# Kernel optimization log

Measured on AMD Instinct MI355X. Metric: run time of the kernel, lower is better.

Reference implementation:

```python
import jax, jax.numpy as jnp
import numpy as np

N, B, T, D = 4, 4, 512, 512
H, DK, DV = 8, 64, 64
LN_EPS = 1e-5


def setup_inputs() -> dict:
    key = jax.random.key(0)
    ks = jax.random.split(key, 5)
    s = 1.0 / np.sqrt(D)
    return {
        "x": jax.random.normal(ks[0], (N, B, T, D), jnp.float32),
        "Wq": jax.random.normal(ks[1], (D, H * DK), jnp.float32) * s,
        "bq": jnp.zeros((H * DK,), jnp.float32),
        "Wk": jax.random.normal(ks[2], (D, H * DK), jnp.float32) * s,
        "bk": jnp.zeros((H * DK,), jnp.float32),
        "Wv": jax.random.normal(ks[3], (D, H * DV), jnp.float32) * s,
        "bv": jnp.zeros((H * DV,), jnp.float32),
        "Wo": jax.random.normal(ks[4], (H * DV, D), jnp.float32) * (1.0 / np.sqrt(H * DV)),
        "bo": jnp.zeros((D,), jnp.float32),
        "gamma": jnp.ones((D,), jnp.float32),
        "beta": jnp.zeros((D,), jnp.float32),
    }


def reference(x, Wq, bq, Wk, bk, Wv, bv, Wo, bo, gamma, beta):
    # x: [N, B, T, D] -- N variables, each [B, T, D]
    n = x.shape[0]
    # Project once per variable (the torch code redundantly recomputes K/V per query var).
    q = (x @ Wq + bq).reshape(n, B, T, H, DK).transpose(0, 1, 3, 2, 4)  # [N,B,H,T,DK]
    k = (x @ Wk + bk).reshape(n, B, T, H, DK).transpose(0, 1, 3, 2, 4)  # [N,B,H,T,DK]
    v = (x @ Wv + bv).reshape(n, B, T, H, DV).transpose(0, 1, 3, 2, 4)  # [N,B,H,T,DV]
    # All-pairs attention: softmax over keys of EACH key-variable separately.
    scores = jnp.einsum('qbhtk,cbhsk->qcbhts', q, k) / np.sqrt(DK)  # [Nq,Nc,B,H,T,T]
    attn = jax.nn.softmax(scores, axis=-1)
    ctx = jnp.einsum('qcbhts,cbhsv->qcbhtv', attn, v)  # [Nq,Nc,B,H,T,DV]
    ctx = ctx.transpose(0, 1, 2, 4, 3, 5).reshape(n, n, B, T, H * DV)
    out = ctx @ Wo + bo                     # per-pair output projection
    out = out.sum(axis=1) / n               # average over key variables -> [N,B,T,D]
    res = x + out
    mu = res.mean(axis=-1, keepdims=True)
    var = res.var(axis=-1, keepdims=True)
    y = (res - mu) / jnp.sqrt(var + LN_EPS) * gamma + beta
    return y
```

## Files before the change

### kernel.cpp

```cpp
#include <hip/hip_runtime.h>


typedef __bf16 bf16x8 __attribute__((ext_vector_type(8)));
typedef __bf16 bf16x4 __attribute__((ext_vector_type(4)));
typedef short shortx4 __attribute__((ext_vector_type(4)));
typedef float floatx4 __attribute__((ext_vector_type(4)));
typedef float floatx16 __attribute__((ext_vector_type(16)));
typedef unsigned short ushortx8 __attribute__((ext_vector_type(8)));

static __device__ __forceinline__ unsigned short f2bf(float f) {
  union { __bf16 h; unsigned short u; } c; c.h = (__bf16)f; return c.u;
}
static __device__ __forceinline__ float bf2f(unsigned short u) {
  union { unsigned u32; float f; } c; c.u32 = ((unsigned)u) << 16; return c.f;
}

#define QSCALE 0.18033688011112042f
#define SHIFT2 (-17.312340489609306f)

__global__ __launch_bounds__(256) void prep(
    const float* __restrict__ Wq, const float* __restrict__ Wk,
    const float* __restrict__ Wv, const float* __restrict__ Wo,
    const float* __restrict__ x,
    unsigned short* __restrict__ wqkvT, unsigned short* __restrict__ woT,
    unsigned short* __restrict__ x_bf)
{
  const int bid = blockIdx.x;
  const int tid = threadIdx.x;
  if (bid < 256) {
    __shared__ unsigned short lds[64][65];
    const int z = bid >> 6, rest = bid & 63;
    const int k0 = (rest >> 3) * 64, n0 = (rest & 7) * 64;
    const float* W; unsigned short* T;
    if (z == 0)      { W = Wq; T = wqkvT; }
    else if (z == 1) { W = Wk; T = wqkvT + 262144; }
    else if (z == 2) { W = Wv; T = wqkvT + 524288; }
    else             { W = Wo; T = woT; }
    const int xx = tid & 63, yy = tid >> 6;
#pragma unroll
    for (int i = 0; i < 16; ++i) {
      const int row = yy * 16 + i;
      lds[row][xx] = f2bf(W[(size_t)(k0 + row) * 512 + n0 + xx]);
    }
    __syncthreads();
#pragma unroll
    for (int i = 0; i < 16; ++i) {
      const int nr = yy * 16 + i;
      T[(size_t)(n0 + nr) * 512 + k0 + xx] = lds[xx][nr];
    }
  } else {
    const int i = (bid - 256) * 256 + tid;
    const float4 a = ((const float4*)x)[i * 2];
    const float4 b = ((const float4*)x)[i * 2 + 1];
    ushortx8 o;
    o[0] = f2bf(a.x); o[1] = f2bf(a.y); o[2] = f2bf(a.z); o[3] = f2bf(a.w);
    o[4] = f2bf(b.x); o[5] = f2bf(b.y); o[6] = f2bf(b.z); o[7] = f2bf(b.w);
    *(ushortx8*)(x_bf + (size_t)i * 8) = o;
  }
}

__global__ __launch_bounds__(256) void gemm_qkv(
    const unsigned short* __restrict__ Xb,
    const unsigned short* __restrict__ BT,
    const float* __restrict__ bq, const float* __restrict__ bk,
    const float* __restrict__ bv,
    unsigned short* __restrict__ Qo, unsigned short* __restrict__ Ko,
    unsigned short* __restrict__ Vo)
{
  __shared__ __align__(16) unsigned short lA[128][72];
  __shared__ __align__(16) unsigned short lB[128][72];
  const int tid  = threadIdx.x;
  const int wv   = tid >> 6, lane = tid & 63;
  const int quad = lane >> 4, l16 = lane & 15;
  const int wm = wv >> 1, wn = wv & 1;
  const int m0  = blockIdx.x * 128;
  const int by  = blockIdx.y;
  const int n0g = by * 128;
  const int sel = by >> 2;
  const float* bias = (sel == 0) ? bq : (sel == 1) ? bk : bv;
  const float scale = (sel == 0) ? QSCALE : 1.0f;
  unsigned short* outp = (sel == 0) ? Qo : (sel == 1) ? Ko : Vo;

  floatx4 acc[4][4] = {};
  const int srow = tid >> 1, sc0 = (tid & 1) * 32;

  for (int kc = 0; kc < 512; kc += 64) {
    __syncthreads();
    const unsigned short* as = Xb + (size_t)(m0 + srow) * 512 + kc + sc0;
    const unsigned short* bs = BT + (size_t)(n0g + srow) * 512 + kc + sc0;
#pragma unroll
    for (int j = 0; j < 4; ++j) {
      *(bf16x8*)&lA[srow][sc0 + j * 8] = *(const bf16x8*)(as + j * 8);
      *(bf16x8*)&lB[srow][sc0 + j * 8] = *(const bf16x8*)(bs + j * 8);
    }
    __syncthreads();
    bf16x8 af[4][2];
#pragma unroll
    for (int ti = 0; ti < 4; ++ti) {
      af[ti][0] = *(const bf16x8*)&lA[wm * 64 + ti * 16 + l16][quad * 8];
      af[ti][1] = *(const bf16x8*)&lA[wm * 64 + ti * 16 + l16][32 + quad * 8];
    }
#pragma unroll
    for (int ni = 0; ni < 4; ++ni) {
      bf16x8 b0 = *(const bf16x8*)&lB[wn * 64 + ni * 16 + l16][quad * 8];
      bf16x8 b1 = *(const bf16x8*)&lB[wn * 64 + ni * 16 + l16][32 + quad * 8];
#pragma unroll
      for (int ti = 0; ti < 4; ++ti) {
        acc[ti][ni] = __builtin_amdgcn_mfma_f32_16x16x32_bf16(af[ti][0], b0, acc[ti][ni], 0, 0, 0);
        acc[ti][ni] = __builtin_amdgcn_mfma_f32_16x16x32_bf16(af[ti][1], b1, acc[ti][ni], 0, 0, 0);
      }
    }
  }

#pragma unroll
  for (int ni = 0; ni < 4; ++ni) {
    const int n = (n0g & 511) + wn * 64 + ni * 16 + l16;
    const float bvv = bias[n];
    const int hh = n >> 6, dk = n & 63;
#pragma unroll
    for (int ti = 0; ti < 4; ++ti) {
      const int mb = m0 + wm * 64 + ti * 16 + quad * 4;
#pragma unroll
      for (int r = 0; r < 4; ++r) {
        const int m = mb + r;
        const int nb = m >> 9, t = m & 511;
        const float v = (acc[ti][ni][r] + bvv) * scale;
        if (sel == 2)
          outp[((size_t)(nb * 8 + hh) * 64 + dk) * 512 + t] = f2bf(v);
        else
          outp[((size_t)(nb * 8 + hh) * 512 + t) * 64 + dk] = f2bf(v);
      }
    }
  }
}

__global__ __launch_bounds__(256) void gemm_out(
    const unsigned short* __restrict__ C0, const unsigned short* __restrict__ C1,
    const unsigned short* __restrict__ BT, float* __restrict__ Cout)
{
  __shared__ __align__(16) unsigned short lA[128][72];
  __shared__ __align__(16) unsigned short lB[128][72];
  const int tid  = threadIdx.x;
  const int wv   = tid >> 6, lane = tid & 63;
  const int quad = lane >> 4, l16 = lane & 15;
  const int wm = wv >> 1, wn = wv & 1;
  const int m0 = blockIdx.x * 128, n0 = blockIdx.y * 128;

  floatx4 acc[4][4] = {};
  const int srow = tid >> 1, sc0 = (tid & 1) * 32;

  for (int kc = 0; kc < 512; kc += 64) {
    __syncthreads();
    const size_t aoff = (size_t)(m0 + srow) * 512 + kc + sc0;
    const unsigned short* bs = BT + (size_t)(n0 + srow) * 512 + kc + sc0;
#pragma unroll
    for (int j = 0; j < 4; ++j) {
      ushortx8 a0 = *(const ushortx8*)(C0 + aoff + j * 8);
      ushortx8 a1 = *(const ushortx8*)(C1 + aoff + j * 8);
      ushortx8 o;
#pragma unroll
      for (int e = 0; e < 8; ++e) o[e] = f2bf(bf2f(a0[e]) + bf2f(a1[e]));
      *(ushortx8*)&lA[srow][sc0 + j * 8] = o;
      *(bf16x8*)&lB[srow][sc0 + j * 8] = *(const bf16x8*)(bs + j * 8);
    }
    __syncthreads();
    bf16x8 af[4][2];
#pragma unroll
    for (int ti = 0; ti < 4; ++ti) {
      af[ti][0] = *(const bf16x8*)&lA[wm * 64 + ti * 16 + l16][quad * 8];
      af[ti][1] = *(const bf16x8*)&lA[wm * 64 + ti * 16 + l16][32 + quad * 8];
    }
#pragma unroll
    for (int ni = 0; ni < 4; ++ni) {
      bf16x8 b0 = *(const bf16x8*)&lB[wn * 64 + ni * 16 + l16][quad * 8];
      bf16x8 b1 = *(const bf16x8*)&lB[wn * 64 + ni * 16 + l16][32 + quad * 8];
#pragma unroll
      for (int ti = 0; ti < 4; ++ti) {
        acc[ti][ni] = __builtin_amdgcn_mfma_f32_16x16x32_bf16(af[ti][0], b0, acc[ti][ni], 0, 0, 0);
        acc[ti][ni] = __builtin_amdgcn_mfma_f32_16x16x32_bf16(af[ti][1], b1, acc[ti][ni], 0, 0, 0);
      }
    }
  }

#pragma unroll
  for (int ni = 0; ni < 4; ++ni) {
    const int n = n0 + wn * 64 + ni * 16 + l16;
#pragma unroll
    for (int ti = 0; ti < 4; ++ti) {
      const int mb = m0 + wm * 64 + ti * 16 + quad * 4;
#pragma unroll
      for (int r = 0; r < 4; ++r)
        Cout[(size_t)(mb + r) * 512 + n] = acc[ti][ni][r];
    }
  }
}

__global__ __launch_bounds__(256) void flash_kernel(
    const unsigned short* __restrict__ Q,
    const unsigned short* __restrict__ K,
    const unsigned short* __restrict__ VT,
    unsigned short* __restrict__ CTX2)
{
  __shared__ __align__(16) unsigned short lK[2][64][72];
  __shared__ __align__(16) unsigned short lV[2][64][68];
  const int tid  = threadIdx.x;
  const int wv   = tid >> 6, lane = tid & 63;
  const int l32  = lane & 31, u = lane >> 5;

  const int lin  = blockIdx.x;
  const int xcd  = lin & 7, slot = lin >> 3;
  const int tile = slot & 3;
  const int nbh  = xcd * 16 + ((slot >> 2) & 15);
  const int cg   = slot >> 6;
  const int t0   = tile * 128;
  const int h = nbh & 7, nb = nbh >> 3, b = nb & 3;

  const unsigned short* qbase = Q + ((size_t)nbh * 512 + (t0 + wv * 32 + l32)) * 64;
  bf16x8 qf[4];
#pragma unroll
  for (int c16 = 0; c16 < 4; ++c16)
    qf[c16] = *(const bf16x8*)(qbase + c16 * 16 + u * 8);

  const int srow = tid >> 2, sc0 = (tid & 3) * 16;
  const unsigned short *kptr, *vptr;
  auto setptr = [&](int it) {
    const int c = cg * 2 + (it >> 3), s0 = (it & 7) * 64;
    const size_t kvbh = (size_t)((c * 4 + b) * 8 + h);
    kptr = K  + kvbh * (512 * 64) + (size_t)(s0 + srow) * 64 + sc0;
    vptr = VT + kvbh * (64 * 512) + (size_t)srow * 512 + s0 + sc0;
  };
  bf16x8 rk0, rk1, rv0, rv1;
  auto loadregs = [&]() {
    rk0 = *(const bf16x8*)kptr; rk1 = *(const bf16x8*)(kptr + 8);
    rv0 = *(const bf16x8*)vptr; rv1 = *(const bf16x8*)(vptr + 8);
  };
  auto writebuf = [&](int p) {
    *(bf16x8*)&lK[p][srow][sc0]     = rk0;
    *(bf16x8*)&lK[p][srow][sc0 + 8] = rk1;
    union { bf16x8 v8; bf16x4 v4[2]; } c0, c1;
    c0.v8 = rv0; c1.v8 = rv1;
    *(bf16x4*)&lV[p][srow][sc0]      = c0.v4[0];
    *(bf16x4*)&lV[p][srow][sc0 + 4]  = c0.v4[1];
    *(bf16x4*)&lV[p][srow][sc0 + 8]  = c1.v4[0];
    *(bf16x4*)&lV[p][srow][sc0 + 12] = c1.v4[1];
  };

  setptr(0); loadregs();
  writebuf(0);
  setptr(1); loadregs();
  __syncthreads();

  floatx16 ofin0 = {}, ofin1 = {};
  floatx16 oc0, oc1;
  float lacc;

  for (int it = 0; it < 16; ++it) {
    const int cur = it & 1;
    const int st = it & 7;
    if (st == 0) { oc0 = floatx16{}; oc1 = floatx16{}; lacc = 0.f; }

    if (it < 15) writebuf(cur ^ 1);
    if (it < 14) { setptr(it + 2); loadregs(); }

    floatx16 sacc0, sacc1;
#pragma unroll
    for (int r = 0; r < 16; ++r) { sacc0[r] = SHIFT2; sacc1[r] = SHIFT2; }
#pragma unroll
    for (int c16 = 0; c16 < 4; ++c16) {
      bf16x8 ak0 = *(const bf16x8*)&lK[cur][l32][c16 * 16 + u * 8];
      bf16x8 ak1 = *(const bf16x8*)&lK[cur][32 + l32][c16 * 16 + u * 8];
      sacc0 = __builtin_amdgcn_mfma_f32_32x32x16_bf16(ak0, qf[c16], sacc0, 0, 0, 0);
      sacc1 = __builtin_amdgcn_mfma_f32_32x32x16_bf16(ak1, qf[c16], sacc1, 0, 0, 0);
    }

#pragma unroll
    for (int sb = 0; sb < 2; ++sb) {
      const floatx16& sa = sb ? sacc1 : sacc0;
#pragma unroll
      for (int c8 = 0; c8 < 4; ++c8) {
        float e0 = __builtin_amdgcn_exp2f(sa[4 * c8 + 0]);
        float e1 = __builtin_amdgcn_exp2f(sa[4 * c8 + 1]);
        float e2 = __builtin_amdgcn_exp2f(sa[4 * c8 + 2]);
        float e3 = __builtin_amdgcn_exp2f(sa[4 * c8 + 3]);
        lacc += (e0 + e1) + (e2 + e3);
        shortx4 pf;
        pf[0] = (short)f2bf(e0); pf[1] = (short)f2bf(e1);
        pf[2] = (short)f2bf(e2); pf[3] = (short)f2bf(e3);
        const int sloc = sb * 32 + c8 * 8 + u * 4;
        shortx4 vf0 = *(const shortx4*)&lV[cur][l32][sloc];
        shortx4 vf1 = *(const shortx4*)&lV[cur][32 + l32][sloc];
        oc0 = __builtin_amdgcn_mfma_f32_32x32x8bf16_1k(pf, vf0, oc0, 0, 0, 0);
        oc1 = __builtin_amdgcn_mfma_f32_32x32x8bf16_1k(pf, vf1, oc1, 0, 0, 0);
      }
    }

    if (st == 7) {
      float s = lacc;
      s += __shfl_xor(s, 32);
      const float inv = 1.0f / s;
#pragma unroll
      for (int r = 0; r < 16; ++r) {
        const int trow = (r & 3) + 8 * (r >> 2) + 4 * u;
        const float invr = __shfl(inv, trow);
        ofin0[r] += oc0[r] * invr;
        ofin1[r] += oc1[r] * invr;
      }
    }
    __syncthreads();
  }

  unsigned short* outp = CTX2 + (size_t)cg * (8192 * 512);
  const int mbase = nb * 512 + t0 + wv * 32;
#pragma unroll
  for (int r = 0; r < 16; ++r) {
    const int trow = (r & 3) + 8 * (r >> 2) + 4 * u;
    const size_t rowoff = (size_t)(mbase + trow) * 512 + h * 64;
    outp[rowoff + l32]      = f2bf(ofin0[r]);
    outp[rowoff + 32 + l32] = f2bf(ofin1[r]);
  }
}

__global__ __launch_bounds__(256) void ln_kernel(
    const float* __restrict__ x, const float* __restrict__ tmp,
    const float* __restrict__ bo, const float* __restrict__ gamma,
    const float* __restrict__ beta, float* __restrict__ out)
{
  const int row = blockIdx.x;
  const int t = threadIdx.x;
  const size_t base = (size_t)row * 512;
  const float r0 = x[base + t]       + 0.25f * tmp[base + t]       + bo[t];
  const float r1 = x[base + t + 256] + 0.25f * tmp[base + t + 256] + bo[t + 256];
  float s = r0 + r1, sq = r0 * r0 + r1 * r1;
#pragma unroll
  for (int off = 1; off < 64; off <<= 1) {
    s  += __shfl_xor(s, off);
    sq += __shfl_xor(sq, off);
  }
  __shared__ float ls[4], lq[4];
  const int wv = t >> 6, lane = t & 63;
  if (lane == 0) { ls[wv] = s; lq[wv] = sq; }
  __syncthreads();
  s  = ls[0] + ls[1] + ls[2] + ls[3];
  sq = lq[0] + lq[1] + lq[2] + lq[3];
  const float mu  = s * (1.0f / 512.0f);
  const float var = sq * (1.0f / 512.0f) - mu * mu;
  const float inv = rsqrtf(var + 1e-5f);
  out[base + t]       = (r0 - mu) * inv * gamma[t]       + beta[t];
  out[base + t + 256] = (r1 - mu) * inv * gamma[t + 256] + beta[t + 256];
}

extern "C" void kernel_launch(void* const* d_in, const int* in_sizes, int n_in,
                              void* d_out, int out_size, void* d_ws, size_t ws_size,
                              hipStream_t stream) {
  const float* x     = (const float*)d_in[0];
  const float* Wq    = (const float*)d_in[1];
  const float* bq    = (const float*)d_in[2];
  const float* Wk    = (const float*)d_in[3];
  const float* bk    = (const float*)d_in[4];
  const float* Wv    = (const float*)d_in[5];
  const float* bv    = (const float*)d_in[6];
  const float* Wo    = (const float*)d_in[7];
  const float* bo    = (const float*)d_in[8];
  const float* gamma = (const float*)d_in[9];
  const float* beta  = (const float*)d_in[10];
  float* out = (float*)d_out;

  char* w = (char*)d_ws;
  unsigned short* q_bf  = (unsigned short*)(w);
  unsigned short* k_bf  = (unsigned short*)(w + (size_t)8  * 1024 * 1024);
  unsigned short* vt_bf = (unsigned short*)(w + (size_t)16 * 1024 * 1024);
  unsigned short* x_bf  = (unsigned short*)(w + (size_t)24 * 1024 * 1024);
  unsigned short* ctx2  = (unsigned short*)(w + (size_t)24 * 1024 * 1024);
  unsigned short* wqkvT = (unsigned short*)(w + (size_t)40 * 1024 * 1024);
  unsigned short* woT   = wqkvT + 786432;
  float* tmp            = (float*)(w);

  prep<<<2304, 256, 0, stream>>>(Wq, Wk, Wv, Wo, x, wqkvT, woT, x_bf);
  gemm_qkv<<<dim3(64, 12), 256, 0, stream>>>(x_bf, wqkvT, bq, bk, bv,
                                             q_bf, k_bf, vt_bf);
  flash_kernel<<<1024, 256, 0, stream>>>(q_bf, k_bf, vt_bf, ctx2);
  gemm_out<<<dim3(64, 4), 256, 0, stream>>>(ctx2, ctx2 + (size_t)8192 * 512,
                                            woT, tmp);
  ln_kernel<<<8192, 256, 0, stream>>>(x, tmp, bo, gamma, beta, out);
}
```

Measured before the change: 197.6 us.

## Use direct global-to-LDS loads with XOR swizzle in flash kernel, vectorize layernorm

The flash kernel now stages K/V tiles with global_load_lds straight into unpadded, XOR-swizzled LDS buffers, replacing the register round-trip and its padding. The per-variable-pair context is written out after each phase and read back for accumulation instead of held in registers, which frees registers (launch bounds now ask for 4 blocks) at the cost of extra global traffic. The layernorm kernel moves to one wavefront per row with float4 loads and no shared-memory reduction. There is also a small index cleanup in gemm_qkv. Risks: the direct-to-LDS path has no explicit wait before the barrier, and the bf16 round-trip of the partial sum adds rounding error.

```diff
diff --git a/kernel.cpp b/kernel.cpp
--- a/kernel.cpp
+++ b/kernel.cpp
@@ -2,7 +2,6 @@
 
 
 typedef __bf16 bf16x8 __attribute__((ext_vector_type(8)));
-typedef __bf16 bf16x4 __attribute__((ext_vector_type(4)));
 typedef short shortx4 __attribute__((ext_vector_type(4)));
 typedef float floatx4 __attribute__((ext_vector_type(4)));
 typedef float floatx16 __attribute__((ext_vector_type(16)));
@@ -13,6 +12,12 @@
 }
 static __device__ __forceinline__ float bf2f(unsigned short u) {
   union { unsigned u32; float f; } c; c.u32 = ((unsigned)u) << 16; return c.f;
+}
+
+static __device__ __forceinline__ void gload16(const unsigned short* gp, unsigned short* lp) {
+  __builtin_amdgcn_global_load_lds(
+      (const __attribute__((address_space(1))) unsigned int*)gp,
+      (__attribute__((address_space(3))) unsigned int*)lp, 16, 0, 0);
 }
 
 #define QSCALE 0.18033688011112042f
@@ -74,9 +79,8 @@
   const int quad = lane >> 4, l16 = lane & 15;
   const int wm = wv >> 1, wn = wv & 1;
   const int m0  = blockIdx.x * 128;
-  const int by  = blockIdx.y;
-  const int n0g = by * 128;
-  const int sel = by >> 2;
+  const int n0g = blockIdx.y * 128;
+  const int sel = n0g >> 9;
   const float* bias = (sel == 0) ? bq : (sel == 1) ? bk : bv;
   const float scale = (sel == 0) ? QSCALE : 1.0f;
   unsigned short* outp = (sel == 0) ? Qo : (sel == 1) ? Ko : Vo;
@@ -195,14 +199,14 @@
   }
 }
 
-__global__ __launch_bounds__(256) void flash_kernel(
+__global__ __launch_bounds__(256, 4) void flash_kernel(
     const unsigned short* __restrict__ Q,
     const unsigned short* __restrict__ K,
     const unsigned short* __restrict__ VT,
     unsigned short* __restrict__ CTX2)
 {
-  __shared__ __align__(16) unsigned short lK[2][64][72];
-  __shared__ __align__(16) unsigned short lV[2][64][68];
+  __shared__ __align__(16) unsigned short lK[2][64][64];
+  __shared__ __align__(16) unsigned short lV[2][64][64];
   const int tid  = threadIdx.x;
   const int wv   = tid >> 6, lane = tid & 63;
   const int l32  = lane & 31, u = lane >> 5;
@@ -221,54 +225,44 @@
   for (int c16 = 0; c16 < 4; ++c16)
     qf[c16] = *(const bf16x8*)(qbase + c16 * 16 + u * 8);
 
-  const int srow = tid >> 2, sc0 = (tid & 3) * 16;
-  const unsigned short *kptr, *vptr;
-  auto setptr = [&](int it) {
+  const int lrow8 = lane >> 3;
+  const int glog  = (lane & 7) ^ lrow8;
+  const int m7    = l32 & 7;
+
+  auto issue = [&](int it, int p) {
     const int c = cg * 2 + (it >> 3), s0 = (it & 7) * 64;
     const size_t kvbh = (size_t)((c * 4 + b) * 8 + h);
-    kptr = K  + kvbh * (512 * 64) + (size_t)(s0 + srow) * 64 + sc0;
-    vptr = VT + kvbh * (64 * 512) + (size_t)srow * 512 + s0 + sc0;
+    const unsigned short* kb = K  + kvbh * (512 * 64) + (size_t)s0 * 64;
+    const unsigned short* vb = VT + kvbh * (64 * 512) + s0;
+#pragma unroll
+    for (int j = 0; j < 2; ++j) {
+      const int r8 = wv * 16 + j * 8;
+      gload16(kb + (size_t)(r8 + lrow8) * 64  + glog * 8, &lK[p][r8][0]);
+      gload16(vb + (size_t)(r8 + lrow8) * 512 + glog * 8, &lV[p][r8][0]);
+    }
   };
-  bf16x8 rk0, rk1, rv0, rv1;
-  auto loadregs = [&]() {
-    rk0 = *(const bf16x8*)kptr; rk1 = *(const bf16x8*)(kptr + 8);
-    rv0 = *(const bf16x8*)vptr; rv1 = *(const bf16x8*)(vptr + 8);
-  };
-  auto writebuf = [&](int p) {
-    *(bf16x8*)&lK[p][srow][sc0]     = rk0;
-    *(bf16x8*)&lK[p][srow][sc0 + 8] = rk1;
-    union { bf16x8 v8; bf16x4 v4[2]; } c0, c1;
-    c0.v8 = rv0; c1.v8 = rv1;
-    *(bf16x4*)&lV[p][srow][sc0]      = c0.v4[0];
-    *(bf16x4*)&lV[p][srow][sc0 + 4]  = c0.v4[1];
-    *(bf16x4*)&lV[p][srow][sc0 + 8]  = c1.v4[0];
-    *(bf16x4*)&lV[p][srow][sc0 + 12] = c1.v4[1];
-  };
-
-  setptr(0); loadregs();
-  writebuf(0);
-  setptr(1); loadregs();
+
+  issue(0, 0);
   __syncthreads();
 
-  floatx16 ofin0 = {}, ofin1 = {};
-  floatx16 oc0, oc1;
-  float lacc;
+  floatx16 oc0 = {}, oc1 = {};
+  float lacc = 0.f;
 
   for (int it = 0; it < 16; ++it) {
     const int cur = it & 1;
     const int st = it & 7;
     if (st == 0) { oc0 = floatx16{}; oc1 = floatx16{}; lacc = 0.f; }
 
-    if (it < 15) writebuf(cur ^ 1);
-    if (it < 14) { setptr(it + 2); loadregs(); }
+    if (it < 15) issue(it + 1, cur ^ 1);
 
     floatx16 sacc0, sacc1;
 #pragma unroll
     for (int r = 0; r < 16; ++r) { sacc0[r] = SHIFT2; sacc1[r] = SHIFT2; }
 #pragma unroll
     for (int c16 = 0; c16 < 4; ++c16) {
-      bf16x8 ak0 = *(const bf16x8*)&lK[cur][l32][c16 * 16 + u * 8];
-      bf16x8 ak1 = *(const bf16x8*)&lK[cur][32 + l32][c16 * 16 + u * 8];
+      const int pc = ((c16 * 2 + u) ^ m7) * 8;
+      bf16x8 ak0 = *(const bf16x8*)&lK[cur][l32][pc];
+      bf16x8 ak1 = *(const bf16x8*)&lK[cur][32 + l32][pc];
       sacc0 = __builtin_amdgcn_mfma_f32_32x32x16_bf16(ak0, qf[c16], sacc0, 0, 0, 0);
       sacc1 = __builtin_amdgcn_mfma_f32_32x32x16_bf16(ak1, qf[c16], sacc1, 0, 0, 0);
     }
@@ -286,9 +280,9 @@
         shortx4 pf;
         pf[0] = (short)f2bf(e0); pf[1] = (short)f2bf(e1);
         pf[2] = (short)f2bf(e2); pf[3] = (short)f2bf(e3);
-        const int sloc = sb * 32 + c8 * 8 + u * 4;
-        shortx4 vf0 = *(const shortx4*)&lV[cur][l32][sloc];
-        shortx4 vf1 = *(const shortx4*)&lV[cur][32 + l32][sloc];
+        const int pv = ((sb * 4 + c8) ^ m7) * 8 + u * 4;
+        shortx4 vf0 = *(const shortx4*)&lV[cur][l32][pv];
+        shortx4 vf1 = *(const shortx4*)&lV[cur][32 + l32][pv];
         oc0 = __builtin_amdgcn_mfma_f32_32x32x8bf16_1k(pf, vf0, oc0, 0, 0, 0);
         oc1 = __builtin_amdgcn_mfma_f32_32x32x8bf16_1k(pf, vf1, oc1, 0, 0, 0);
       }
@@ -298,25 +292,24 @@
       float s = lacc;
       s += __shfl_xor(s, 32);
       const float inv = 1.0f / s;
+      unsigned short* outp = CTX2 + (size_t)cg * (8192 * 512);
+      const int mbase = nb * 512 + t0 + wv * 32;
+      const int phase = it >> 3;
 #pragma unroll
       for (int r = 0; r < 16; ++r) {
         const int trow = (r & 3) + 8 * (r >> 2) + 4 * u;
         const float invr = __shfl(inv, trow);
-        ofin0[r] += oc0[r] * invr;
-        ofin1[r] += oc1[r] * invr;
-      }
-    }
-    __syncthreads();
-  }
-
-  unsigned short* outp = CTX2 + (size_t)cg * (8192 * 512);
-  const int mbase = nb * 512 + t0 + wv * 32;
-#pragma unroll
-  for (int r = 0; r < 16; ++r) {
-    const int trow = (r & 3) + 8 * (r >> 2) + 4 * u;
-    const size_t rowoff = (size_t)(mbase + trow) * 512 + h * 64;
-    outp[rowoff + l32]      = f2bf(ofin0[r]);
-    outp[rowoff + 32 + l32] = f2bf(ofin1[r]);
+        const size_t rowoff = (size_t)(mbase + trow) * 512 + h * 64;
+        float v0 = oc0[r] * invr, v1 = oc1[r] * invr;
+        if (phase == 1) {
+          v0 += bf2f(outp[rowoff + l32]);
+          v1 += bf2f(outp[rowoff + 32 + l32]);
+        }
+        outp[rowoff + l32]      = f2bf(v0);
+        outp[rowoff + 32 + l32] = f2bf(v1);
+      }
+    }
+    __syncthreads();
   }
 }
 
@@ -325,28 +318,43 @@
     const float* __restrict__ bo, const float* __restrict__ gamma,
     const float* __restrict__ beta, float* __restrict__ out)
 {
-  const int row = blockIdx.x;
-  const int t = threadIdx.x;
-  const size_t base = (size_t)row * 512;
-  const float r0 = x[base + t]       + 0.25f * tmp[base + t]       + bo[t];
-  const float r1 = x[base + t + 256] + 0.25f * tmp[base + t + 256] + bo[t + 256];
-  float s = r0 + r1, sq = r0 * r0 + r1 * r1;
+  const int wv   = threadIdx.x >> 6, lane = threadIdx.x & 63;
+  const int row  = blockIdx.x * 4 + wv;
+  const int col  = lane * 8;
+  const size_t base = (size_t)row * 512 + col;
+  const float4 x0 = *(const float4*)(x + base);
+  const float4 x1 = *(const float4*)(x + base + 4);
+  const float4 t0 = *(const float4*)(tmp + base);
+  const float4 t1 = *(const float4*)(tmp + base + 4);
+  const float4 b0 = *(const float4*)(bo + col);
+  const float4 b1 = *(const float4*)(bo + col + 4);
+  float r[8];
+  r[0] = x0.x + 0.25f * t0.x + b0.x;  r[1] = x0.y + 0.25f * t0.y + b0.y;
+  r[2] = x0.z + 0.25f * t0.z + b0.z;  r[3] = x0.w + 0.25f * t0.w + b0.w;
+  r[4] = x1.x + 0.25f * t1.x + b1.x;  r[5] = x1.y + 0.25f * t1.y + b1.y;
+  r[6] = x1.z + 0.25f * t1.z + b1.z;  r[7] = x1.w + 0.25f * t1.w + b1.w;
+  float s = 0.f, sq = 0.f;
+#pragma unroll
+  for (int j = 0; j < 8; ++j) { s += r[j]; sq += r[j] * r[j]; }
 #pragma unroll
   for (int off = 1; off < 64; off <<= 1) {
     s  += __shfl_xor(s, off);
     sq += __shfl_xor(sq, off);
   }
-  __shared__ float ls[4], lq[4];
-  const int wv = t >> 6, lane = t & 63;
-  if (lane == 0) { ls[wv] = s; lq[wv] = sq; }
-  __syncthreads();
-  s  = ls[0] + ls[1] + ls[2] + ls[3];
-  sq = lq[0] + lq[1] + lq[2] + lq[3];
   const float mu  = s * (1.0f / 512.0f);
   const float var = sq * (1.0f / 512.0f) - mu * mu;
   const float inv = rsqrtf(var + 1e-5f);
-  out[base + t]       = (r0 - mu) * inv * gamma[t]       + beta[t];
-  out[base + t + 256] = (r1 - mu) * inv * gamma[t + 256] + beta[t + 256];
+  const float4 g0 = *(const float4*)(gamma + col);
+  const float4 g1 = *(const float4*)(gamma + col + 4);
+  const float4 be0 = *(const float4*)(beta + col);
+  const float4 be1 = *(const float4*)(beta + col + 4);
+  float4 o0, o1;
+  o0.x = (r[0] - mu) * inv * g0.x + be0.x;  o0.y = (r[1] - mu) * inv * g0.y + be0.y;
+  o0.z = (r[2] - mu) * inv * g0.z + be0.z;  o0.w = (r[3] - mu) * inv * g0.w + be0.w;
+  o1.x = (r[4] - mu) * inv * g1.x + be1.x;  o1.y = (r[5] - mu) * inv * g1.y + be1.y;
+  o1.z = (r[6] - mu) * inv * g1.z + be1.z;  o1.w = (r[7] - mu) * inv * g1.w + be1.w;
+  *(float4*)(out + base)     = o0;
+  *(float4*)(out + base + 4) = o1;
 }
 
 extern "C" void kernel_launch(void* const* d_in, const int* in_sizes, int n_in,
@@ -381,5 +389,5 @@
   flash_kernel<<<1024, 256, 0, stream>>>(q_bf, k_bf, vt_bf, ctx2);
   gemm_out<<<dim3(64, 4), 256, 0, stream>>>(ctx2, ctx2 + (size_t)8192 * 512,
                                             woT, tmp);
-  ln_kernel<<<8192, 256, 0, stream>>>(x, tmp, bo, gamma, beta, out);
-}
+  ln_kernel<<<2048, 256, 0, stream>>>(x, tmp, bo, gamma, beta, out);
+}
```

After: 250.0 us. +26.5%, slower.

## Stage V transpose through LDS, store projection output in bf16, vectorize layernorm

Applied to the files above, without the earlier changes.

The V branch of the QKV GEMM now transposes its tile through shared memory and writes coalesced 16-byte rows, replacing strided scalar stores. The output-projection GEMM writes its intermediate in bf16 instead of fp32, halving that buffer's write and read traffic. The layernorm is rewritten so one wavefront handles one row with vectorized loads and stores and no block-level sync. The bf16 intermediate adds rounding error before the residual add and layernorm.

```diff
diff --git a/kernel.cpp b/kernel.cpp
--- a/kernel.cpp
+++ b/kernel.cpp
@@ -67,16 +67,16 @@
     unsigned short* __restrict__ Qo, unsigned short* __restrict__ Ko,
     unsigned short* __restrict__ Vo)
 {
-  __shared__ __align__(16) unsigned short lA[128][72];
-  __shared__ __align__(16) unsigned short lB[128][72];
+  __shared__ __align__(16) unsigned short sbuf[18432];
+  auto lA = (unsigned short (*)[72])sbuf;
+  auto lB = (unsigned short (*)[72])(sbuf + 9216);
   const int tid  = threadIdx.x;
   const int wv   = tid >> 6, lane = tid & 63;
   const int quad = lane >> 4, l16 = lane & 15;
   const int wm = wv >> 1, wn = wv & 1;
   const int m0  = blockIdx.x * 128;
-  const int by  = blockIdx.y;
-  const int n0g = by * 128;
-  const int sel = by >> 2;
+  const int n0g = blockIdx.y * 128;
+  const int sel = n0g >> 9;
   const float* bias = (sel == 0) ? bq : (sel == 1) ? bk : bv;
   const float scale = (sel == 0) ? QSCALE : 1.0f;
   unsigned short* outp = (sel == 0) ? Qo : (sel == 1) ? Ko : Vo;
@@ -112,31 +112,58 @@
     }
   }
 
-#pragma unroll
-  for (int ni = 0; ni < 4; ++ni) {
-    const int n = (n0g & 511) + wn * 64 + ni * 16 + l16;
-    const float bvv = bias[n];
+  if (sel != 2) {
+#pragma unroll
+    for (int ni = 0; ni < 4; ++ni) {
+      const int n = (n0g & 511) + wn * 64 + ni * 16 + l16;
+      const float bvv = bias[n];
+      const int hh = n >> 6, dk = n & 63;
+#pragma unroll
+      for (int ti = 0; ti < 4; ++ti) {
+        const int mb = m0 + wm * 64 + ti * 16 + quad * 4;
+#pragma unroll
+        for (int r = 0; r < 4; ++r) {
+          const int m = mb + r;
+          const int nb = m >> 9, t = m & 511;
+          outp[((size_t)(nb * 8 + hh) * 512 + t) * 64 + dk] =
+              f2bf((acc[ti][ni][r] + bvv) * scale);
+        }
+      }
+    }
+  } else {
+    __syncthreads();
+    auto tb = (unsigned short (*)[136])sbuf;
+#pragma unroll
+    for (int ni = 0; ni < 4; ++ni) {
+      const int n = (n0g & 511) + wn * 64 + ni * 16 + l16;
+      const float bvv = bias[n];
+      const int drow = wn * 64 + ni * 16 + l16;
+#pragma unroll
+      for (int ti = 0; ti < 4; ++ti) {
+        const int tcol = wm * 64 + ti * 16 + quad * 4;
+        shortx4 pk;
+        pk[0] = (short)f2bf(acc[ti][ni][0] + bvv);
+        pk[1] = (short)f2bf(acc[ti][ni][1] + bvv);
+        pk[2] = (short)f2bf(acc[ti][ni][2] + bvv);
+        pk[3] = (short)f2bf(acc[ti][ni][3] + bvv);
+        *(shortx4*)&tb[drow][tcol] = pk;
+      }
+    }
+    __syncthreads();
+    const int drow = tid >> 1, th = tid & 1;
+    const int n = (n0g & 511) + drow;
     const int hh = n >> 6, dk = n & 63;
-#pragma unroll
-    for (int ti = 0; ti < 4; ++ti) {
-      const int mb = m0 + wm * 64 + ti * 16 + quad * 4;
-#pragma unroll
-      for (int r = 0; r < 4; ++r) {
-        const int m = mb + r;
-        const int nb = m >> 9, t = m & 511;
-        const float v = (acc[ti][ni][r] + bvv) * scale;
-        if (sel == 2)
-          outp[((size_t)(nb * 8 + hh) * 64 + dk) * 512 + t] = f2bf(v);
-        else
-          outp[((size_t)(nb * 8 + hh) * 512 + t) * 64 + dk] = f2bf(v);
-      }
-    }
+    const int nb = m0 >> 9, tbase = (m0 & 511) + th * 64;
+    unsigned short* gdst = outp + ((size_t)(nb * 8 + hh) * 64 + dk) * 512 + tbase;
+#pragma unroll
+    for (int j = 0; j < 8; ++j)
+      *(ushortx8*)(gdst + j * 8) = *(const ushortx8*)&tb[drow][th * 64 + j * 8];
   }
 }
 
 __global__ __launch_bounds__(256) void gemm_out(
     const unsigned short* __restrict__ C0, const unsigned short* __restrict__ C1,
-    const unsigned short* __restrict__ BT, float* __restrict__ Cout)
+    const unsigned short* __restrict__ BT, unsigned short* __restrict__ Cout)
 {
   __shared__ __align__(16) unsigned short lA[128][72];
   __shared__ __align__(16) unsigned short lB[128][72];
@@ -190,7 +217,7 @@
       const int mb = m0 + wm * 64 + ti * 16 + quad * 4;
 #pragma unroll
       for (int r = 0; r < 4; ++r)
-        Cout[(size_t)(mb + r) * 512 + n] = acc[ti][ni][r];
+        Cout[(size_t)(mb + r) * 512 + n] = f2bf(acc[ti][ni][r]);
     }
   }
 }
@@ -321,32 +348,46 @@
 }
 
 __global__ __launch_bounds__(256) void ln_kernel(
-    const float* __restrict__ x, const float* __restrict__ tmp,
+    const float* __restrict__ x, const unsigned short* __restrict__ tmpb,
     const float* __restrict__ bo, const float* __restrict__ gamma,
     const float* __restrict__ beta, float* __restrict__ out)
 {
-  const int row = blockIdx.x;
-  const int t = threadIdx.x;
-  const size_t base = (size_t)row * 512;
-  const float r0 = x[base + t]       + 0.25f * tmp[base + t]       + bo[t];
-  const float r1 = x[base + t + 256] + 0.25f * tmp[base + t + 256] + bo[t + 256];
-  float s = r0 + r1, sq = r0 * r0 + r1 * r1;
+  const int wv   = threadIdx.x >> 6, lane = threadIdx.x & 63;
+  const int row  = blockIdx.x * 4 + wv;
+  const int col  = lane * 8;
+  const size_t base = (size_t)row * 512 + col;
+  const float4 x0 = *(const float4*)(x + base);
+  const float4 x1 = *(const float4*)(x + base + 4);
+  const ushortx8 t8 = *(const ushortx8*)(tmpb + base);
+  const float4 b0 = *(const float4*)(bo + col);
+  const float4 b1 = *(const float4*)(bo + col + 4);
+  float r[8];
+  r[0] = x0.x + 0.25f * bf2f(t8[0]) + b0.x;  r[1] = x0.y + 0.25f * bf2f(t8[1]) + b0.y;
+  r[2] = x0.z + 0.25f * bf2f(t8[2]) + b0.z;  r[3] = x0.w + 0.25f * bf2f(t8[3]) + b0.w;
+  r[4] = x1.x + 0.25f * bf2f(t8[4]) + b1.x;  r[5] = x1.y + 0.25f * bf2f(t8[5]) + b1.y;
+  r[6] = x1.z + 0.25f * bf2f(t8[6]) + b1.z;  r[7] = x1.w + 0.25f * bf2f(t8[7]) + b1.w;
+  float s = 0.f, sq = 0.f;
+#pragma unroll
+  for (int j = 0; j < 8; ++j) { s += r[j]; sq += r[j] * r[j]; }
 #pragma unroll
   for (int off = 1; off < 64; off <<= 1) {
     s  += __shfl_xor(s, off);
     sq += __shfl_xor(sq, off);
   }
-  __shared__ float ls[4], lq[4];
-  const int wv = t >> 6, lane = t & 63;
-  if (lane == 0) { ls[wv] = s; lq[wv] = sq; }
-  __syncthreads();
-  s  = ls[0] + ls[1] + ls[2] + ls[3];
-  sq = lq[0] + lq[1] + lq[2] + lq[3];
   const float mu  = s * (1.0f / 512.0f);
   const float var = sq * (1.0f / 512.0f) - mu * mu;
   const float inv = rsqrtf(var + 1e-5f);
-  out[base + t]       = (r0 - mu) * inv * gamma[t]       + beta[t];
-  out[base + t + 256] = (r1 - mu) * inv * gamma[t + 256] + beta[t + 256];
+  const float4 g0 = *(const float4*)(gamma + col);
+  const float4 g1 = *(const float4*)(gamma + col + 4);
+  const float4 be0 = *(const float4*)(beta + col);
+  const float4 be1 = *(const float4*)(beta + col + 4);
+  float4 o0, o1;
+  o0.x = (r[0] - mu) * inv * g0.x + be0.x;  o0.y = (r[1] - mu) * inv * g0.y + be0.y;
+  o0.z = (r[2] - mu) * inv * g0.z + be0.z;  o0.w = (r[3] - mu) * inv * g0.w + be0.w;
+  o1.x = (r[4] - mu) * inv * g1.x + be1.x;  o1.y = (r[5] - mu) * inv * g1.y + be1.y;
+  o1.z = (r[6] - mu) * inv * g1.z + be1.z;  o1.w = (r[7] - mu) * inv * g1.w + be1.w;
+  *(float4*)(out + base)     = o0;
+  *(float4*)(out + base + 4) = o1;
 }
 
 extern "C" void kernel_launch(void* const* d_in, const int* in_sizes, int n_in,
@@ -373,13 +414,13 @@
   unsigned short* ctx2  = (unsigned short*)(w + (size_t)24 * 1024 * 1024);
   unsigned short* wqkvT = (unsigned short*)(w + (size_t)40 * 1024 * 1024);
   unsigned short* woT   = wqkvT + 786432;
-  float* tmp            = (float*)(w);
+  unsigned short* tmpb  = (unsigned short*)(w);
 
   prep<<<2304, 256, 0, stream>>>(Wq, Wk, Wv, Wo, x, wqkvT, woT, x_bf);
   gemm_qkv<<<dim3(64, 12), 256, 0, stream>>>(x_bf, wqkvT, bq, bk, bv,
                                              q_bf, k_bf, vt_bf);
   flash_kernel<<<1024, 256, 0, stream>>>(q_bf, k_bf, vt_bf, ctx2);
   gemm_out<<<dim3(64, 4), 256, 0, stream>>>(ctx2, ctx2 + (size_t)8192 * 512,
-                                            woT, tmp);
-  ln_kernel<<<8192, 256, 0, stream>>>(x, tmp, bo, gamma, beta, out);
-}
+                                            woT, tmpb);
+  ln_kernel<<<2048, 256, 0, stream>>>(x, tmpb, bo, gamma, beta, out);
+}
```

Result: no change. 195.5 us (-1.1%).
